# Kernel optimization log

Hardware: AMD Instinct MI355X
Metric: run time of the kernel (lower is better)

## Reference

```python
import jax, jax.numpy as jnp
import numpy as np

N_NODES = 50000
N_EDGES = 800000
IN_C = 128
HID = 64          # hidden_channels
OUT_C = 128


def _glorot(key, shape):
    fan_in, fan_out = shape[1], shape[0]
    lim = (6.0 / (fan_in + fan_out)) ** 0.5
    return jax.random.uniform(key, shape, jnp.float32, -lim, lim)


def setup_inputs() -> dict:
    key = jax.random.key(0)
    ks = jax.random.split(key, 12)
    x = jax.random.normal(ks[0], (N_NODES, IN_C), jnp.float32)
    edge_index = jax.random.randint(ks[1], (2, N_EDGES), 0, N_NODES, jnp.int64)
    # SAGEConv params: lin_l (aggregated neighbors, with bias), lin_r (self, no bias)
    # layer1: 128 -> 128 (hidden*2), layer2: 128 -> 64, layer3: 64 -> 128
    d1, d2, d3 = 2 * HID, HID, OUT_C
    return {
        "x": x,
        "edge_index": edge_index,
        "W1l": _glorot(ks[2], (d1, IN_C)), "b1": jnp.zeros((d1,), jnp.float32), "W1r": _glorot(ks[3], (d1, IN_C)),
        "W2l": _glorot(ks[4], (d2, d1)),  "b2": jnp.zeros((d2,), jnp.float32), "W2r": _glorot(ks[5], (d2, d1)),
        "W3l": _glorot(ks[6], (d3, d2)),  "b3": jnp.zeros((d3,), jnp.float32), "W3r": _glorot(ks[7], (d3, d2)),
    }


def _sage_conv(x, src, dst, Wl, bl, Wr):
    # mean-aggregate source features at destination nodes (PyG SAGEConv, aggr='mean')
    msg = x[src]                                                  # [E, d]
    agg = jax.ops.segment_sum(msg, dst, num_segments=N_NODES)     # [N, d]
    cnt = jax.ops.segment_sum(jnp.ones((src.shape[0],), x.dtype), dst, num_segments=N_NODES)
    mean = agg / jnp.maximum(cnt, 1.0)[:, None]
    return mean @ Wl.T + bl + x @ Wr.T


def reference(x, edge_index, W1l, b1, W1r, W2l, b2, W2r, W3l, b3, W3r):
    src, dst = edge_index[0], edge_index[1]
    h1 = jax.nn.relu(_sage_conv(x, src, dst, W1l, b1, W1r))   # dropout: eval mode -> identity
    h2 = jax.nn.relu(_sage_conv(h1, src, dst, W2l, b2, W2r))
    h3 = jax.nn.relu(_sage_conv(h2, src, dst, W3l, b3, W3r))
    return jnp.concatenate([h1, h2, h3], axis=1)              # torch.hstack
```

## Files before the change

### kernel.cpp

```cpp
#include <hip/hip_runtime.h>
#include <hip/hip_bf16.h>

#define N_NODES 50000
#define N_EDGES 800000

constexpr int NP = 50176;

typedef __attribute__((ext_vector_type(8))) short bf16x8;
typedef __attribute__((ext_vector_type(4))) float f32x4;

__device__ __forceinline__ unsigned short f2bf(float f) {
    unsigned u = __float_as_uint(f);
    u += 0x7FFFu + ((u >> 16) & 1u);
    return (unsigned short)(u >> 16);
}

__global__ void count_kernel(const int* __restrict__ dst, int* __restrict__ cnt,
                             int* __restrict__ pos, int E) {
    int i = blockIdx.x * blockDim.x + threadIdx.x;
    if (i < E) pos[i] = atomicAdd(&cnt[dst[i]], 1);
}

__global__ void assign_kernel(const int* __restrict__ cnt, int* __restrict__ row_ptr,
                              float* __restrict__ inv_deg, int* __restrict__ total, int n) {
    int i = blockIdx.x * blockDim.x + threadIdx.x;
    int lane = threadIdx.x & 63;
    int v = (i < n) ? cnt[i] : 0;
    int s = v;
    #pragma unroll
    for (int off = 1; off < 64; off <<= 1) {
        int t = __shfl_up(s, off);
        if (lane >= off) s += t;
    }
    int base = 0;
    if (lane == 63) base = atomicAdd(total, s);
    base = __shfl(base, 63);
    if (i < n) {
        row_ptr[i] = base + s - v;
        inv_deg[i] = 1.0f / (float)(v > 1 ? v : 1);
    }
}

__global__ void fill_kernel(const int* __restrict__ src, const int* __restrict__ dst,
                            const int* __restrict__ row_ptr, const int* __restrict__ pos,
                            int* __restrict__ edge_src, int E) {
    int i = blockIdx.x * blockDim.x + threadIdx.x;
    if (i < E) edge_src[row_ptr[dst[i]] + pos[i]] = src[i];
}

__global__ void build_wcat_kernel(const float* __restrict__ Wl, const float* __restrict__ Wr,
                                  unsigned short* __restrict__ Wc, int din, int dout) {
    int idx = blockIdx.x * blockDim.x + threadIdx.x;
    int K = 2 * din;
    if (idx >= dout * K) return;
    int nrow = idx / K;
    int k = idx - nrow * K;
    float v = (k < din) ? Wl[nrow * din + k] : Wr[nrow * din + (k - din)];
    Wc[idx] = f2bf(v);
}

__global__ void cvt_kernel(const float* __restrict__ src, unsigned short* __restrict__ dstb, int total4) {
    int i = blockIdx.x * blockDim.x + threadIdx.x;
    if (i >= total4) return;
    float4 v = reinterpret_cast<const float4*>(src)[i];
    uint2 p;
    p.x = (unsigned)f2bf(v.x) | ((unsigned)f2bf(v.y) << 16);
    p.y = (unsigned)f2bf(v.z) | ((unsigned)f2bf(v.w) << 16);
    reinterpret_cast<uint2*>(dstb)[i] = p;
}

template<int D>
__global__ __launch_bounds__(256) void agg_kernel(
        const unsigned short* __restrict__ hb,
        const int* __restrict__ row_ptr, const int* __restrict__ cnt,
        const int* __restrict__ edge_src,
        const float* __restrict__ inv_deg, unsigned short* __restrict__ meanb, int n) {
    constexpr int LPR = D / 8;
    constexpr int EPW = 64 / LPR;
    int wid = (blockIdx.x * 256 + threadIdx.x) >> 6;
    int lane = threadIdx.x & 63;
    if (wid >= n) return;
    int beg = row_ptr[wid];
    int end = beg + cnt[wid];
    float inv = inv_deg[wid];
    int sub = lane / LPR;
    int li = lane % LPR;

    float acc[8];
    #pragma unroll
    for (int j = 0; j < 8; ++j) acc[j] = 0.f;

    for (int e0 = beg; e0 < end; e0 += 2 * EPW) {
        int e = e0 + sub;
        int e2 = e + EPW;
        uint4 v0 = {0u, 0u, 0u, 0u}, v1 = {0u, 0u, 0u, 0u};
        if (e < end) {
            int s0 = edge_src[e];
            v0 = *reinterpret_cast<const uint4*>(hb + (size_t)s0 * D + li * 8);
        }
        if (e2 < end) {
            int s1 = edge_src[e2];
            v1 = *reinterpret_cast<const uint4*>(hb + (size_t)s1 * D + li * 8);
        }
        unsigned w;
        #define ACCW(u, j0) w = (u); acc[j0] += __uint_as_float(w << 16); acc[j0+1] += __uint_as_float(w & 0xFFFF0000u)
        ACCW(v0.x, 0); ACCW(v0.y, 2); ACCW(v0.z, 4); ACCW(v0.w, 6);
        ACCW(v1.x, 0); ACCW(v1.y, 2); ACCW(v1.z, 4); ACCW(v1.w, 6);
        #undef ACCW
    }
    #pragma unroll
    for (int off = LPR; off < 64; off <<= 1) {
        #pragma unroll
        for (int j = 0; j < 8; ++j) acc[j] += __shfl_xor(acc[j], off);
    }
    if (lane < LPR) {
        uint4 w;
        w.x = (unsigned)f2bf(acc[0] * inv) | ((unsigned)f2bf(acc[1] * inv) << 16);
        w.y = (unsigned)f2bf(acc[2] * inv) | ((unsigned)f2bf(acc[3] * inv) << 16);
        w.z = (unsigned)f2bf(acc[4] * inv) | ((unsigned)f2bf(acc[5] * inv) << 16);
        w.w = (unsigned)f2bf(acc[6] * inv) | ((unsigned)f2bf(acc[7] * inv) << 16);
        *reinterpret_cast<uint4*>(meanb + (size_t)wid * D + li * 8) = w;
    }
}

template<int K, int DOUT, bool WB>
__global__ __launch_bounds__(256, 3) void mfma_gemm_kernel(
        const unsigned short* __restrict__ Ab,
        const unsigned short* __restrict__ Fb,
        const unsigned short* __restrict__ Wc,
        const float* __restrict__ bias,
        float* __restrict__ out, int outs,
        unsigned short* __restrict__ outb, int n) {
    constexpr int DIN = K / 2;
    constexpr int NT = DOUT / 16;
    constexpr int KK = K / 32;
    int wave = threadIdx.x >> 6;
    int lane = threadIdx.x & 63;
    int m0 = blockIdx.x * 64 + wave * 16;
    int arow = lane & 15;
    int kseg = lane >> 4;
    int node = m0 + arow;
    int nc = (node < n) ? node : 0;

    bf16x8 a[KK];
    #pragma unroll
    for (int kk = 0; kk < KK; ++kk) {
        int k = kk * 32 + kseg * 8;
        const unsigned short* p = (k < DIN) ? (Ab + (size_t)nc * DIN + k)
                                            : (Fb + (size_t)nc * DIN + (k - DIN));
        a[kk] = *reinterpret_cast<const bf16x8*>(p);
    }

    f32x4 acc[NT];
    #pragma unroll
    for (int t = 0; t < NT; ++t) acc[t] = {0.f, 0.f, 0.f, 0.f};

    const unsigned short* wbase = Wc + (size_t)arow * K + kseg * 8;
    #pragma unroll
    for (int kk = 0; kk < KK; ++kk) {
        bf16x8 b[NT];
        #pragma unroll
        for (int t = 0; t < NT; ++t)
            b[t] = *reinterpret_cast<const bf16x8*>(wbase + (size_t)t * 16 * K + kk * 32);
        #pragma unroll
        for (int t = 0; t < NT; ++t)
            acc[t] = __builtin_amdgcn_mfma_f32_16x16x32_bf16(a[kk], b[t], acc[t], 0, 0, 0);
    }

    int crow0 = m0 + kseg * 4;
    #pragma unroll
    for (int r = 0; r < 4; ++r) {
        int gn = crow0 + r;
        if (gn < n) {
            #pragma unroll
            for (int t = 0; t < NT; ++t) {
                int col = t * 16 + arow;
                float v = fmaxf(acc[t][r] + bias[col], 0.f);
                out[(size_t)gn * outs + col] = v;
                if constexpr (WB) outb[(size_t)gn * DOUT + col] = f2bf(v);
            }
        }
    }
}

extern "C" void kernel_launch(void* const* d_in, const int* in_sizes, int n_in,
                              void* d_out, int out_size, void* d_ws, size_t ws_size,
                              hipStream_t stream) {
    const float* x   = (const float*)d_in[0];
    const int*   ei  = (const int*)d_in[1];
    const float* W1l = (const float*)d_in[2];
    const float* b1  = (const float*)d_in[3];
    const float* W1r = (const float*)d_in[4];
    const float* W2l = (const float*)d_in[5];
    const float* b2  = (const float*)d_in[6];
    const float* W2r = (const float*)d_in[7];
    const float* W3l = (const float*)d_in[8];
    const float* b3  = (const float*)d_in[9];
    const float* W3r = (const float*)d_in[10];
    float* out = (float*)d_out;

    const int* src = ei;
    const int* dst = ei + N_EDGES;

    int* wsi = (int*)d_ws;
    int*   cnt      = wsi;
    int*   total    = wsi + NP;
    int*   row_ptr  = wsi + NP + 64;
    float* inv_deg  = (float*)(wsi + 2 * NP + 64);
    int*   edge_src = wsi + 3 * NP + 64;
    int*   pos      = edge_src + N_EDGES;
    unsigned short* Wc1 = (unsigned short*)(pos + N_EDGES);
    unsigned short* Wc2 = Wc1 + 128 * 256;
    unsigned short* Wc3 = Wc2 + 64 * 256;
    unsigned short* meanb = Wc3 + 128 * 128;
    unsigned short* featb = meanb + (size_t)N_NODES * 128;
    unsigned short* h2b   = featb + (size_t)N_NODES * 128;

    hipMemsetAsync(cnt, 0, (size_t)(NP + 64) * 4, stream);

    const int EB = (N_EDGES + 255) / 256;
    count_kernel<<<EB, 256, 0, stream>>>(dst, cnt, pos, N_EDGES);
    assign_kernel<<<NP / 256, 256, 0, stream>>>(cnt, row_ptr, inv_deg, total, N_NODES);
    fill_kernel<<<EB, 256, 0, stream>>>(src, dst, row_ptr, pos, edge_src, N_EDGES);

    build_wcat_kernel<<<(128 * 256 + 255) / 256, 256, 0, stream>>>(W1l, W1r, Wc1, 128, 128);
    build_wcat_kernel<<<(64 * 256 + 255) / 256, 256, 0, stream>>>(W2l, W2r, Wc2, 128, 64);
    build_wcat_kernel<<<(128 * 128 + 255) / 256, 256, 0, stream>>>(W3l, W3r, Wc3, 64, 128);

    cvt_kernel<<<(N_NODES * 128 / 4 + 255) / 256, 256, 0, stream>>>(x, featb, N_NODES * 128 / 4);

    const int AGG_BLOCKS = (N_NODES + 3) / 4;
    const int GEMM_BLOCKS = (N_NODES + 63) / 64;

    agg_kernel<128><<<AGG_BLOCKS, 256, 0, stream>>>(featb, row_ptr, cnt, edge_src, inv_deg, meanb, N_NODES);
    mfma_gemm_kernel<256, 128, true><<<GEMM_BLOCKS, 256, 0, stream>>>(meanb, featb, Wc1, b1, out, 320, featb, N_NODES);

    agg_kernel<128><<<AGG_BLOCKS, 256, 0, stream>>>(featb, row_ptr, cnt, edge_src, inv_deg, meanb, N_NODES);
    mfma_gemm_kernel<256, 64, true><<<GEMM_BLOCKS, 256, 0, stream>>>(meanb, featb, Wc2, b2, out + 128, 320, h2b, N_NODES);

    agg_kernel<64><<<AGG_BLOCKS, 256, 0, stream>>>(h2b, row_ptr, cnt, edge_src, inv_deg, meanb, N_NODES);
    mfma_gemm_kernel<128, 128, false><<<GEMM_BLOCKS, 256, 0, stream>>>(meanb, h2b, Wc3, b3, out + 192, 320, nullptr, N_NODES);
}
```

Before: 255.1 us.

## Restructure MFMA GEMM to keep weight slice in registers and double-buffer A tiles

Each wave now owns a 32-column slice of the output and keeps its weight fragments in registers for the whole block. It loops over four 16-row groups, double-buffering the A-operand loads so the next group's load overlaps the current MFMAs. Blocks now cover 64 or 128 rows depending on DOUT, so weight reloads per row drop. Layer 1 also writes its bf16 output to a separate buffer instead of the input buffer it reads, which removes an in-place read/write race. Register pressure rises under launch_bounds(256,3).

```diff
diff --git a/kernel.cpp b/kernel.cpp
--- a/kernel.cpp
+++ b/kernel.cpp
@@ -132,55 +132,84 @@
         float* __restrict__ out, int outs,
         unsigned short* __restrict__ outb, int n) {
     constexpr int DIN = K / 2;
-    constexpr int NT = DOUT / 16;
     constexpr int KK = K / 32;
+    constexpr int NWC = DOUT / 32;
+    constexpr int NWM = 4 / NWC;
+    constexpr int GW = 4;
+    constexpr int BM = 16 * GW * NWM;
     int wave = threadIdx.x >> 6;
     int lane = threadIdx.x & 63;
-    int m0 = blockIdx.x * 64 + wave * 16;
+    int wc = wave % NWC;
+    int wm = wave / NWC;
     int arow = lane & 15;
     int kseg = lane >> 4;
-    int node = m0 + arow;
-    int nc = (node < n) ? node : 0;
-
-    bf16x8 a[KK];
-    #pragma unroll
-    for (int kk = 0; kk < KK; ++kk) {
-        int k = kk * 32 + kseg * 8;
-        const unsigned short* p = (k < DIN) ? (Ab + (size_t)nc * DIN + k)
-                                            : (Fb + (size_t)nc * DIN + (k - DIN));
-        a[kk] = *reinterpret_cast<const bf16x8*>(p);
-    }
-
-    f32x4 acc[NT];
-    #pragma unroll
-    for (int t = 0; t < NT; ++t) acc[t] = {0.f, 0.f, 0.f, 0.f};
-
-    const unsigned short* wbase = Wc + (size_t)arow * K + kseg * 8;
-    #pragma unroll
-    for (int kk = 0; kk < KK; ++kk) {
-        bf16x8 b[NT];
+
+    bf16x8 b0[KK], b1[KK];
+    {
+        const unsigned short* wp0 = Wc + (size_t)(wc * 32 + arow) * K + kseg * 8;
+        const unsigned short* wp1 = wp0 + (size_t)16 * K;
         #pragma unroll
-        for (int t = 0; t < NT; ++t)
-            b[t] = *reinterpret_cast<const bf16x8*>(wbase + (size_t)t * 16 * K + kk * 32);
-        #pragma unroll
-        for (int t = 0; t < NT; ++t)
-            acc[t] = __builtin_amdgcn_mfma_f32_16x16x32_bf16(a[kk], b[t], acc[t], 0, 0, 0);
-    }
-
-    int crow0 = m0 + kseg * 4;
-    #pragma unroll
-    for (int r = 0; r < 4; ++r) {
-        int gn = crow0 + r;
-        if (gn < n) {
-            #pragma unroll
-            for (int t = 0; t < NT; ++t) {
-                int col = t * 16 + arow;
-                float v = fmaxf(acc[t][r] + bias[col], 0.f);
-                out[(size_t)gn * outs + col] = v;
-                if constexpr (WB) outb[(size_t)gn * DOUT + col] = f2bf(v);
-            }
+        for (int kk = 0; kk < KK; ++kk) {
+            b0[kk] = *reinterpret_cast<const bf16x8*>(wp0 + kk * 32);
+            b1[kk] = *reinterpret_cast<const bf16x8*>(wp1 + kk * 32);
         }
     }
+    float bv0 = bias[wc * 32 + arow];
+    float bv1 = bias[wc * 32 + 16 + arow];
+
+    int g0 = blockIdx.x * (BM / 16) + wm * GW;
+
+    bf16x8 a0[KK], a1[KK];
+
+    #define LOADA(g, dst)                                                          \
+    {                                                                              \
+        int node = (g0 + (g)) * 16 + arow;                                         \
+        int ncl = node < n ? node : 0;                                             \
+        _Pragma("unroll")                                                          \
+        for (int kk = 0; kk < KK; ++kk) {                                          \
+            int k = kk * 32 + kseg * 8;                                            \
+            const unsigned short* p = (k < DIN) ? (Ab + (size_t)ncl * DIN + k)     \
+                                                : (Fb + (size_t)ncl * DIN + (k - DIN)); \
+            dst[kk] = *reinterpret_cast<const bf16x8*>(p);                         \
+        }                                                                          \
+    }
+
+    #define COMPUTE(g, ab)                                                         \
+    {                                                                              \
+        f32x4 acc0 = {0.f, 0.f, 0.f, 0.f}, acc1 = {0.f, 0.f, 0.f, 0.f};           \
+        _Pragma("unroll")                                                          \
+        for (int kk = 0; kk < KK; ++kk) {                                          \
+            acc0 = __builtin_amdgcn_mfma_f32_16x16x32_bf16(ab[kk], b0[kk], acc0, 0, 0, 0); \
+            acc1 = __builtin_amdgcn_mfma_f32_16x16x32_bf16(ab[kk], b1[kk], acc1, 0, 0, 0); \
+        }                                                                          \
+        int gbase = (g0 + (g)) * 16 + kseg * 4;                                    \
+        _Pragma("unroll")                                                          \
+        for (int r = 0; r < 4; ++r) {                                              \
+            int gn = gbase + r;                                                    \
+            if (gn < n) {                                                          \
+                int col0 = wc * 32 + arow;                                         \
+                float v0 = fmaxf(acc0[r] + bv0, 0.f);                              \
+                float v1 = fmaxf(acc1[r] + bv1, 0.f);                              \
+                out[(size_t)gn * outs + col0] = v0;                                \
+                out[(size_t)gn * outs + col0 + 16] = v1;                           \
+                if constexpr (WB) {                                                \
+                    outb[(size_t)gn * DOUT + col0] = f2bf(v0);                     \
+                    outb[(size_t)gn * DOUT + col0 + 16] = f2bf(v1);                \
+                }                                                                  \
+            }                                                                      \
+        }                                                                          \
+    }
+
+    LOADA(0, a0);
+    #pragma unroll
+    for (int gp = 0; gp < GW; gp += 2) {
+        LOADA(gp + 1, a1);
+        COMPUTE(gp, a0);
+        if (gp + 2 < GW) LOADA(gp + 2, a0);
+        COMPUTE(gp + 1, a1);
+    }
+    #undef LOADA
+    #undef COMPUTE
 }
 
 extern "C" void kernel_launch(void* const* d_in, const int* in_sizes, int n_in,
@@ -213,8 +242,9 @@
     unsigned short* Wc2 = Wc1 + 128 * 256;
     unsigned short* Wc3 = Wc2 + 64 * 256;
     unsigned short* meanb = Wc3 + 128 * 128;
-    unsigned short* featb = meanb + (size_t)N_NODES * 128;
-    unsigned short* h2b   = featb + (size_t)N_NODES * 128;
+    unsigned short* xb  = meanb + (size_t)N_NODES * 128;
+    unsigned short* h1b = xb + (size_t)N_NODES * 128;
+    unsigned short* h2b = h1b + (size_t)N_NODES * 128;
 
     hipMemsetAsync(cnt, 0, (size_t)(NP + 64) * 4, stream);
 
@@ -227,17 +257,18 @@
     build_wcat_kernel<<<(64 * 256 + 255) / 256, 256, 0, stream>>>(W2l, W2r, Wc2, 128, 64);
     build_wcat_kernel<<<(128 * 128 + 255) / 256, 256, 0, stream>>>(W3l, W3r, Wc3, 64, 128);
 
-    cvt_kernel<<<(N_NODES * 128 / 4 + 255) / 256, 256, 0, stream>>>(x, featb, N_NODES * 128 / 4);
+    cvt_kernel<<<(N_NODES * 128 / 4 + 255) / 256, 256, 0, stream>>>(x, xb, N_NODES * 128 / 4);
 
     const int AGG_BLOCKS = (N_NODES + 3) / 4;
-    const int GEMM_BLOCKS = (N_NODES + 63) / 64;
-
-    agg_kernel<128><<<AGG_BLOCKS, 256, 0, stream>>>(featb, row_ptr, cnt, edge_src, inv_deg, meanb, N_NODES);
-    mfma_gemm_kernel<256, 128, true><<<GEMM_BLOCKS, 256, 0, stream>>>(meanb, featb, Wc1, b1, out, 320, featb, N_NODES);
-
-    agg_kernel<128><<<AGG_BLOCKS, 256, 0, stream>>>(featb, row_ptr, cnt, edge_src, inv_deg, meanb, N_NODES);
-    mfma_gemm_kernel<256, 64, true><<<GEMM_BLOCKS, 256, 0, stream>>>(meanb, featb, Wc2, b2, out + 128, 320, h2b, N_NODES);
+    const int GB64  = (N_NODES + 63) / 64;
+    const int GB128 = (N_NODES + 127) / 128;
+
+    agg_kernel<128><<<AGG_BLOCKS, 256, 0, stream>>>(xb, row_ptr, cnt, edge_src, inv_deg, meanb, N_NODES);
+    mfma_gemm_kernel<256, 128, true><<<GB64, 256, 0, stream>>>(meanb, xb, Wc1, b1, out, 320, h1b, N_NODES);
+
+    agg_kernel<128><<<AGG_BLOCKS, 256, 0, stream>>>(h1b, row_ptr, cnt, edge_src, inv_deg, meanb, N_NODES);
+    mfma_gemm_kernel<256, 64, true><<<GB128, 256, 0, stream>>>(meanb, h1b, Wc2, b2, out + 128, 320, h2b, N_NODES);
 
     agg_kernel<64><<<AGG_BLOCKS, 256, 0, stream>>>(h2b, row_ptr, cnt, edge_src, inv_deg, meanb, N_NODES);
-    mfma_gemm_kernel<128, 128, false><<<GEMM_BLOCKS, 256, 0, stream>>>(meanb, h2b, Wc3, b3, out + 192, 320, nullptr, N_NODES);
-}
+    mfma_gemm_kernel<128, 128, false><<<GB64, 256, 0, stream>>>(meanb, h2b, Wc3, b3, out + 192, 320, nullptr, N_NODES);
+}
```

Result: faster. 229.9 us (-9.9%).
